# Kernel tuning notes

Measured on AMD Instinct MI355X. Metric: run time of the kernel, lower is better.

Reference implementation:

```python
import jax, jax.numpy as jnp
import numpy as np
from jax import lax

EPS = 1e-10
DELU_P = 10.0

def delu(x):
    # delu_feature_map: param*relu(x) + (exp(param*min(x,0)) - 1) + 1
    x1 = jax.nn.relu(x)
    x2 = jnp.exp(DELU_P * (x - x1)) - 1.0
    return DELU_P * x1 + x2 + 1.0

def conv1x1(x, w, b):
    # x: (B,C,H,W), w: (O,C), b: (O,)
    return jnp.einsum('bchw,oc->bohw', x, w) + b[None, :, None, None]

def conv3x3(x, w, b):
    # w: (O,I,3,3), SAME padding, stride 1
    y = lax.conv_general_dilated(x, w, window_strides=(1, 1), padding='SAME',
                                 dimension_numbers=('NCHW', 'OIHW', 'NCHW'))
    return y + b[None, :, None, None]

def setup_inputs() -> dict:
    key = jax.random.key(0)
    ks = jax.random.split(key, 12)
    B, C, H, W = 4, 256, 128, 128
    s = 0.02
    return {
        'x':   jax.random.normal(ks[0], (B, C, H, W), dtype=jnp.float32),
        'wq':  jax.random.normal(ks[1], (C, C), dtype=jnp.float32) * s,
        'bq':  jax.random.normal(ks[2], (C,), dtype=jnp.float32) * s,
        'wk':  jax.random.normal(ks[3], (C, C), dtype=jnp.float32) * s,
        'bk':  jax.random.normal(ks[4], (C,), dtype=jnp.float32) * s,
        'wv':  jax.random.normal(ks[5], (C, C), dtype=jnp.float32) * s,
        'bv':  jax.random.normal(ks[6], (C,), dtype=jnp.float32) * s,
        'wd1': jax.random.normal(ks[7], (C, C), dtype=jnp.float32) * s,
        'bd1': jax.random.normal(ks[8], (C,), dtype=jnp.float32) * s,
        'wd3': jax.random.normal(ks[9], (C, C, 3, 3), dtype=jnp.float32) * s,
        'bd3': jax.random.normal(ks[10], (C,), dtype=jnp.float32) * s,
        'gamma': jax.random.normal(ks[11], (1,), dtype=jnp.float32) * 0.1,
    }

def reference(x, wq, bq, wk, bk, wv, bv, wd1, bd1, wd3, bd3, gamma):
    B, C, H, W = x.shape
    N = H * W
    # q/k/v projections flattened to (B, C, N)
    q = conv1x1(x, wq, bq).reshape(B, C, N)
    k = conv1x1(x, wk, bk).reshape(B, C, N)
    v = conv1x1(x, wv, bv).reshape(B, C, N)
    # feature maps (torch permutes q to (B,N,C), applies map, permutes back -> elementwise, no-op layout)
    q = delu(q)
    k = delu(k)
    # energy: (B, C, C), contracting over spatial N (q indexed 'bmn')
    energy = jnp.einsum('bmn,bcn->bmc', q, k)
    KV = k * v  # (B, C, N) elementwise
    norm = 1.0 / (jnp.einsum('bmc,bcn->bn', energy, k) + EPS)  # (B, N)
    # attention: sum over m of energy, times KV, times norm -> (B, C, N)
    attention = jnp.einsum('bmc,bcn,bn->bcn', energy, KV, norm)
    out = attention.reshape(B, C, H, W)
    out = out + conv1x1(x, wd1, bd1) + conv3x3(x, wd3, bd3)
    return x + gamma[0] * out
```

## Files before the change

kernel.cpp:

```cpp
#include <hip/hip_runtime.h>
#include <hip/hip_fp8.h>

#define BB 4
#define CC 256
#define HH 128
#define WW 128
#define NN (HH*WW)
#define EPSF 1e-10f

#define XR 130
#define XPB ((size_t)XR*XR*CC)

typedef __bf16 bf16x8 __attribute__((ext_vector_type(8)));
typedef float  f32x4  __attribute__((ext_vector_type(4)));
typedef float  f32x16 __attribute__((ext_vector_type(16)));
typedef unsigned char uchar;

__device__ __forceinline__ float delu_f(float v) {
    return v > 0.0f ? fmaf(10.0f, v, 1.0f) : __expf(10.0f * v);
}

__device__ __forceinline__ uchar fp8b(float f) { return __hip_fp8_e4m3(f).__x; }
__device__ __forceinline__ float fp8f(uchar v) { __hip_fp8_e4m3 t; t.__x = v; return (float)t; }

__device__ __forceinline__ void gl_lds16(const void* g, void* l) {
    __builtin_amdgcn_global_load_lds(
        (const __attribute__((address_space(1))) void*)g,
        (__attribute__((address_space(3))) void*)l, 16, 0, 0);
}

__global__ __launch_bounds__(256) void k_prep(const float* __restrict__ wq,
    const float* __restrict__ wk, const float* __restrict__ wv,
    const float* __restrict__ wd1, const float* __restrict__ wd3,
    __bf16* __restrict__ wqb, __bf16* __restrict__ wkb, __bf16* __restrict__ wvb,
    uchar* __restrict__ wcv8)
{
    int idx = blockIdx.x * 256 + threadIdx.x;
    if (idx >= CC*CC) return;
    const int oc = idx >> 8, ic = idx & 255;
    const int ocf32 = oc >> 5;
    const int gks = ic >> 4, khi = (ic >> 3) & 1;
    const int lane32 = khi*32 + (oc & 31);
    const int e = ic & 7;
    const size_t off32 = ((size_t)(gks*8 + ocf32)*64 + lane32)*8 + e;
    wqb[off32] = (__bf16)wq[idx];
    wkb[off32] = (__bf16)wk[idx];
    wvb[off32] = (__bf16)wv[idx];
    float w9[9];
    #pragma unroll
    for (int k=0;k<9;k++) w9[k] = wd3[(size_t)idx*9 + k];
    w9[4] += wd1[idx];
    #pragma unroll
    for (int t=0;t<9;t++) wcv8[(size_t)t*CC*CC + off32] = fp8b(w9[t] * 16.0f);
}

__global__ __launch_bounds__(256) void k_halo(__bf16* __restrict__ xpad,
                                              uchar* __restrict__ xpad8)
{
    const int b = blockIdx.y;
    for (int t = blockIdx.x*256 + threadIdx.x; t < 516*32; t += 256*gridDim.x) {
        const int icg = t & 31;
        const int p   = t >> 5;
        int xrow, xcol;
        if (p < 260)      { xrow = (p < 130) ? 0 : 129; xcol = p % 130; }
        else              { int q = p - 260; xrow = 1 + (q >> 1); xcol = (q & 1) ? 129 : 0; }
        const size_t off = (size_t)b*XPB + ((size_t)xrow*XR + xcol)*CC + icg*8;
        *(bf16x8*)&xpad[off] = (bf16x8){};
        *(unsigned long long*)&xpad8[off] = 0ull;
    }
}

__global__ __launch_bounds__(256) void k_xpad(const float* __restrict__ x,
                                              __bf16* __restrict__ xpad,
                                              uchar* __restrict__ xpad8)
{
    __shared__ __bf16 tb[256*66];
    const int chunk = blockIdx.x;
    const int hr    = blockIdx.y;
    const int b     = blockIdx.z;
    const int tid   = threadIdx.x;
    const int wc0   = chunk*64;
    const float* xb = x + (size_t)b*CC*NN + (size_t)hr*WW + wc0;

    #pragma unroll
    for (int i = 0; i < 16; ++i) {
        const int ic  = i*16 + (tid >> 4);
        const int wcl = (tid & 15)*4;
        float4 v = *(const float4*)&xb[(size_t)ic*NN + wcl];
        __bf16* d = &tb[ic*66 + wcl];
        d[0] = (__bf16)v.x; d[1] = (__bf16)v.y; d[2] = (__bf16)v.z; d[3] = (__bf16)v.w;
    }
    __syncthreads();

    __bf16* xpb  = xpad  + (size_t)b*XPB + ((size_t)(hr+1)*XR + wc0 + 1)*CC;
    uchar*  xpb8 = xpad8 + (size_t)b*XPB + ((size_t)(hr+1)*XR + wc0 + 1)*CC;
    #pragma unroll
    for (int it = 0; it < 8; ++it) {
        const int o   = it*256 + tid;
        const int col = o >> 5;
        const int ic8 = (o & 31)*8;
        bf16x8 v;
        unsigned long long pk = 0;
        #pragma unroll
        for (int j = 0; j < 8; ++j) {
            __bf16 e = tb[(ic8 + j)*66 + col];
            v[j] = e;
            pk |= ((unsigned long long)fp8b((float)e)) << (8*j);
        }
        *(bf16x8*)&xpb[(size_t)col*CC + ic8] = v;
        *(unsigned long long*)&xpb8[(size_t)col*CC + ic8] = pk;
    }
}

__device__ __forceinline__ void stage_row128(const __bf16* __restrict__ xrb,
                                             __bf16* __restrict__ xs,
                                             int wid, int lane)
{
    #pragma unroll
    for (int j = 0; j < 16; ++j) {
        const int it = wid + 4*j;
        const int kq = it >> 1, ch = it & 1;
        gl_lds16(xrb + (size_t)(ch*64 + lane)*CC + kq*8, &xs[(size_t)(kq*132 + ch*64)*8]);
    }
}

__device__ __forceinline__ void mfma_gemm32(const __bf16* __restrict__ wb,
                                            const __bf16* __restrict__ xs,
                                            int wid, int lane, int l31, int lhi,
                                            f32x16 acc[2][4])
{
    #pragma unroll
    for (int kb=0; kb<8; kb++) {
        bf16x8 af[4];
        #pragma unroll
        for (int f=0; f<2; f++)
            #pragma unroll
            for (int kk=0; kk<2; kk++)
                af[f*2+kk] = *(const bf16x8*)&wb[((size_t)((kb*2+kk)*8 + wid*2 + f)*64 + lane)*8];
        #pragma unroll
        for (int kk=0; kk<2; kk++)
            #pragma unroll
            for (int nf=0; nf<4; nf++) {
                bf16x8 br = *(const bf16x8*)&xs[(size_t)((kb*4 + kk*2 + lhi)*132 + nf*32 + l31)*8];
                #pragma unroll
                for (int f=0; f<2; f++)
                    acc[f][nf] = __builtin_amdgcn_mfma_f32_32x32x16_bf16(af[f*2+kk], br, acc[f][nf], 0, 0, 0);
            }
    }
}

__global__ __launch_bounds__(256) void k_qk_mfma(const __bf16* __restrict__ xpad,
    const __bf16* __restrict__ wqb, const float* __restrict__ bq,
    const __bf16* __restrict__ wkb, const float* __restrict__ bk,
    uchar* __restrict__ kp8, float* __restrict__ Qs)
{
    __shared__ __bf16 xs[32*132*8];
    __shared__ float Qpart[4][128];
    const int h  = blockIdx.x;
    const int n0 = h * 128;
    const int b  = blockIdx.y;
    const int tid = threadIdx.x;
    const int wid = tid >> 6, lane = tid & 63;
    const int l31 = lane & 31, lhi = lane >> 5;
    const int oc_base = wid*64;
    const __bf16* xrb = xpad + (size_t)b*XPB + ((size_t)(h+1)*XR + 1)*CC;

    stage_row128(xrb, xs, wid, lane);
    __syncthreads();

    f32x16 acc[2][4] = {};
    mfma_gemm32(wqb, xs, wid, lane, l31, lhi, acc);
    #pragma unroll
    for (int nf=0; nf<4; nf++) {
        float s = 0.0f;
        #pragma unroll
        for (int f=0; f<2; f++)
            #pragma unroll
            for (int reg=0; reg<16; reg++) {
                const int oc = oc_base + f*32 + (reg&3) + 8*(reg>>2) + 4*lhi;
                s += delu_f(acc[f][nf][reg] + bq[oc]);
            }
        s += __shfl_xor(s, 32);
        if (lhi == 0) Qpart[wid][nf*32 + l31] = s;
    }
    __syncthreads();
    if (tid < 128)
        Qs[(size_t)b*NN + n0 + tid] = Qpart[0][tid] + Qpart[1][tid] + Qpart[2][tid] + Qpart[3][tid];

    #pragma unroll
    for (int f=0; f<2; f++)
        #pragma unroll
        for (int nf=0; nf<4; nf++)
            acc[f][nf] = (f32x16){};
    mfma_gemm32(wkb, xs, wid, lane, l31, lhi, acc);
    #pragma unroll
    for (int f=0; f<2; f++) {
        #pragma unroll
        for (int reg=0; reg<16; reg++) {
            const int oc = oc_base + f*32 + (reg&3) + 8*(reg>>2) + 4*lhi;
            const float bias = bk[oc];
            uchar* kr = kp8 + ((size_t)b*CC + oc)*NN + n0;
            #pragma unroll
            for (int nf=0; nf<4; nf++)
                kr[nf*32 + l31] = fp8b(delu_f(acc[f][nf][reg] + bias));
        }
    }
}

__global__ __launch_bounds__(256) void k_esum(const uchar* __restrict__ kp8,
    const float* __restrict__ Qs, float* __restrict__ Es)
{
    const int c = blockIdx.x & (CC-1), b = blockIdx.x >> 8;
    const int tid = threadIdx.x;
    const uchar* kr = kp8 + ((size_t)b*CC + c)*NN;
    const float4* qr = (const float4*)(Qs + (size_t)b*NN);
    float s = 0.0f;
    for (int i = tid; i < NN/8; i += 256) {
        unsigned long long kkb = *(const unsigned long long*)&kr[(size_t)i*8];
        float4 q0 = qr[2*i], q1 = qr[2*i+1];
        const float qv[8] = {q0.x,q0.y,q0.z,q0.w,q1.x,q1.y,q1.z,q1.w};
        #pragma unroll
        for (int j=0;j<8;j++)
            s = fmaf(fp8f((uchar)(kkb >> (8*j))), qv[j], s);
    }
    #pragma unroll
    for (int m=1; m<64; m<<=1) s += __shfl_xor(s, m, 64);
    __shared__ float red[4];
    if ((tid & 63) == 0) red[tid >> 6] = s;
    __syncthreads();
    if (tid == 0) Es[b*CC + c] = red[0] + red[1] + red[2] + red[3];
}

__global__ __launch_bounds__(256,2) void k_conv_mfma(const uchar* __restrict__ xpad8,
    const uchar* __restrict__ wcv8, const float* __restrict__ bd1,
    const float* __restrict__ bd3, __bf16* __restrict__ convout)
{
    __shared__ uchar xs8[2][6*132*16];
    const int orig = blockIdx.x;
    const int wg   = (orig & 7)*64 + (orig >> 3);
    const int b    = wg >> 7;
    const int h    = wg & 127;
    const int tid = threadIdx.x;
    const int wid = tid >> 6, lane = tid & 63;
    const int l31 = lane & 31, lhi = lane >> 5;
    const int oc_base = wid*64;
    const uchar* xpb8 = xpad8 + (size_t)b*XPB;

    f32x16 acc[2][4] = {};

    #define STAGE_CV8(bufsel, icb) do {                                         \
        const int ic0_ = (icb)*32;                                              \
        _Pragma("unroll")                                                       \
        for (int j = 0; j < 5; ++j) {                                           \
            const int w_ = wid + 4*j;                                           \
            if (w_ < 18) {                                                      \
                const int pair_ = w_ / 3, chunk_ = w_ % 3;                      \
                const int r_ = pair_ >> 1, g16_ = pair_ & 1;                    \
                const int col0_ = chunk_ * 64;                                  \
                if (col0_ + lane < XR)                                          \
                    gl_lds16(xpb8 + ((size_t)(h + r_)*XR + col0_ + lane)*CC + ic0_ + g16_*16, \
                             &xs8[bufsel][(size_t)(pair_*132 + col0_)*16]);     \
            }                                                                   \
        }                                                                       \
    } while (0)

    #define AF8_LOAD(dst, t, icb)                                               \
        _Pragma("unroll")                                                       \
        for (int f=0; f<2; f++)                                                 \
            _Pragma("unroll")                                                   \
            for (int kk=0; kk<2; kk++)                                          \
                dst[f*2+kk] = *(const long*)&wcv8[(size_t)(t)*CC*CC +           \
                    ((size_t)((((icb)*2 + kk)*8 + wid*2 + f))*64 + lane)*8];

    STAGE_CV8(0, 0);
    __syncthreads();

    #pragma unroll 1
    for (int icb = 0; icb < 8; ++icb) {
        long af8[2][4];
        AF8_LOAD(af8[0], 0, icb);
        if (icb < 7) STAGE_CV8((icb+1)&1, icb+1);
        #pragma unroll
        for (int t=0; t<9; ++t) {
            const int cur = t & 1, nxt = cur ^ 1;
            const int ky = t/3, kx = t%3;
            if (t < 8) { AF8_LOAD(af8[nxt], t+1, icb); }
            __builtin_amdgcn_s_setprio(1);
            #pragma unroll
            for (int kk=0; kk<2; kk++) {
                #pragma unroll
                for (int nf=0; nf<4; nf++) {
                    long br = *(const long*)&xs8[icb & 1][
                        (size_t)((ky*2 + kk)*132 + nf*32 + l31 + kx)*16 + lhi*8];
                    #pragma unroll
                    for (int f=0; f<2; f++)
                        acc[f][nf] = __builtin_amdgcn_mfma_f32_32x32x16_fp8_fp8(
                            af8[cur][f*2+kk], br, acc[f][nf], 0, 0, 0);
                }
            }
            __builtin_amdgcn_s_setprio(0);
        }
        __syncthreads();
    }
    #undef STAGE_CV8
    #undef AF8_LOAD

    #pragma unroll
    for (int f=0; f<2; f++) {
        #pragma unroll
        for (int reg=0; reg<16; reg++) {
            const int row = (reg & 3) + 8*(reg >> 2) + 4*lhi;
            const int oc = oc_base + f*32 + row;
            const float bias = bd1[oc] + bd3[oc];
            __bf16* orow = convout + ((size_t)b*CC + oc)*NN + (size_t)h*WW;
            #pragma unroll
            for (int nf=0; nf<4; nf++) {
                const int w = nf*32 + l31;
                orow[w] = (__bf16)(acc[f][nf][reg]*0.0625f + bias);
            }
        }
    }
}

__global__ __launch_bounds__(256) void k_vattn_mfma(
    const __bf16* __restrict__ xpad,
    const __bf16* __restrict__ wvb, const float* __restrict__ bv,
    const uchar* __restrict__ kp8, const float* __restrict__ Es,
    const __bf16* __restrict__ convout,
    const float* __restrict__ gamma, float* __restrict__ out)
{
    __shared__ __bf16 xs[32*132*8];
    __shared__ float Dpart[4][128];
    __shared__ float rn_sh[128];
    const int h  = blockIdx.x;
    const int n0 = h * 128;
    const int b  = blockIdx.y;
    const int tid = threadIdx.x;
    const int wid = tid >> 6, lane = tid & 63;
    const int l31 = lane & 31, lhi = lane >> 5;
    const int oc_base = wid*64;
    const __bf16* xrb = xpad + (size_t)b*XPB + ((size_t)(h+1)*XR + 1)*CC;

    stage_row128(xrb, xs, wid, lane);
    __syncthreads();

    f32x16 acc[2][4] = {};
    mfma_gemm32(wvb, xs, wid, lane, l31, lhi, acc);

    float dpart[4] = {0.f,0.f,0.f,0.f};
    #pragma unroll
    for (int f=0; f<2; f++) {
        #pragma unroll
        for (int reg=0; reg<16; reg++) {
            const int oc = oc_base + f*32 + (reg&3) + 8*(reg>>2) + 4*lhi;
            const float e = Es[b*CC + oc];
            const uchar* kr = kp8 + ((size_t)b*CC + oc)*NN + n0;
            #pragma unroll
            for (int nf=0; nf<4; nf++)
                dpart[nf] = fmaf(e, fp8f(kr[nf*32 + l31]), dpart[nf]);
        }
    }
    #pragma unroll
    for (int nf=0; nf<4; nf++) {
        dpart[nf] += __shfl_xor(dpart[nf], 32);
        if (lhi == 0) Dpart[wid][nf*32 + l31] = dpart[nf];
    }
    __syncthreads();
    if (tid < 128)
        rn_sh[tid] = 1.0f / (Dpart[0][tid] + Dpart[1][tid] + Dpart[2][tid] + Dpart[3][tid] + EPSF);
    __syncthreads();

    const float g = gamma[0];
    #pragma unroll
    for (int f=0; f<2; f++) {
        #pragma unroll
        for (int reg=0; reg<16; reg++) {
            const int oc = oc_base + f*32 + (reg&3) + 8*(reg>>2) + 4*lhi;
            const float eg = Es[b*CC + oc] * g;
            const float bias = bv[oc];
            const uchar*  kr = kp8 + ((size_t)b*CC + oc)*NN + n0;
            const __bf16* cr = convout + ((size_t)b*CC + oc)*NN + n0;
            const __bf16* xr = &xs[(size_t)((oc >> 3)*132)*8 + (oc & 7)];
            float* orow = out + ((size_t)b*CC + oc)*NN + n0;
            #pragma unroll
            for (int nf=0; nf<4; nf++) {
                const int w = nf*32 + l31;
                const float attn = eg*fp8f(kr[w])*rn_sh[w]*(acc[f][nf][reg] + bias);
                const float xv = (float)xr[(size_t)w*8];
                orow[w] = xv + attn + g*(float)cr[w];
            }
        }
    }
}

extern "C" void kernel_launch(void* const* d_in, const int* in_sizes, int n_in,
                              void* d_out, int out_size, void* d_ws, size_t ws_size,
                              hipStream_t stream)
{
    const float* x     = (const float*)d_in[0];
    const float* wq    = (const float*)d_in[1];
    const float* bq    = (const float*)d_in[2];
    const float* wk    = (const float*)d_in[3];
    const float* bk    = (const float*)d_in[4];
    const float* wv    = (const float*)d_in[5];
    const float* bv    = (const float*)d_in[6];
    const float* wd1   = (const float*)d_in[7];
    const float* bd1   = (const float*)d_in[8];
    const float* wd3   = (const float*)d_in[9];
    const float* bd3   = (const float*)d_in[10];
    const float* gamma = (const float*)d_in[11];
    float* out = (float*)d_out;

    uchar*  kp8   = (uchar*)d_ws;
    __bf16* cvout = (__bf16*)(kp8 + (size_t)BB*CC*NN);
    float*  Qs    = (float*)(cvout + (size_t)BB*CC*NN);
    float*  Es    = Qs + (size_t)BB*NN;
    uchar*  wcv8  = (uchar*)(Es + (size_t)BB*CC);
    __bf16* wqb   = (__bf16*)(wcv8 + (size_t)9*CC*CC);
    __bf16* wkb   = wqb + (size_t)CC*CC;
    __bf16* wvb   = wkb + (size_t)CC*CC;
    __bf16* xpad  = wvb + (size_t)CC*CC;
    uchar*  xpad8 = (uchar*)(xpad + (size_t)BB*XPB);

    k_prep      <<<dim3(CC*CC/256), 256, 0, stream>>>(wq, wk, wv, wd1, wd3, wqb, wkb, wvb, wcv8);
    k_halo      <<<dim3(16, BB), 256, 0, stream>>>(xpad, xpad8);
    k_xpad      <<<dim3(2, HH, BB), 256, 0, stream>>>(x, xpad, xpad8);
    k_qk_mfma   <<<dim3(HH, BB), 256, 0, stream>>>(xpad, wqb, bq, wkb, bk, kp8, Qs);
    k_esum      <<<dim3(BB*CC), 256, 0, stream>>>(kp8, Qs, Es);
    k_conv_mfma <<<dim3(HH*BB), 256, 0, stream>>>(xpad8, wcv8, bd1, bd3, cvout);
    k_vattn_mfma<<<dim3(HH, BB), 256, 0, stream>>>(xpad, wvb, bv, kp8, Es, cvout, gamma, out);
}
```

Before: 172.2 us.

## Fuse input transpose/padding into QK projection kernel

Removes the separate k_xpad kernel and has k_qk_mfma read fp32 x directly, convert it to bf16 in LDS in the layout the MFMA GEMM expects, and write the padded bf16 and fp8 copies from LDS for later kernels. This saves one launch and one re-read of the bf16 padded row from global memory. In exchange, the staging uses scattered 2-byte LDS stores that may cause bank conflicts, and it adds global write traffic inside the GEMM kernel.

```diff
diff --git a/kernel.cpp b/kernel.cpp
--- a/kernel.cpp
+++ b/kernel.cpp
@@ -70,48 +70,6 @@
     }
 }
 
-__global__ __launch_bounds__(256) void k_xpad(const float* __restrict__ x,
-                                              __bf16* __restrict__ xpad,
-                                              uchar* __restrict__ xpad8)
-{
-    __shared__ __bf16 tb[256*66];
-    const int chunk = blockIdx.x;
-    const int hr    = blockIdx.y;
-    const int b     = blockIdx.z;
-    const int tid   = threadIdx.x;
-    const int wc0   = chunk*64;
-    const float* xb = x + (size_t)b*CC*NN + (size_t)hr*WW + wc0;
-
-    #pragma unroll
-    for (int i = 0; i < 16; ++i) {
-        const int ic  = i*16 + (tid >> 4);
-        const int wcl = (tid & 15)*4;
-        float4 v = *(const float4*)&xb[(size_t)ic*NN + wcl];
-        __bf16* d = &tb[ic*66 + wcl];
-        d[0] = (__bf16)v.x; d[1] = (__bf16)v.y; d[2] = (__bf16)v.z; d[3] = (__bf16)v.w;
-    }
-    __syncthreads();
-
-    __bf16* xpb  = xpad  + (size_t)b*XPB + ((size_t)(hr+1)*XR + wc0 + 1)*CC;
-    uchar*  xpb8 = xpad8 + (size_t)b*XPB + ((size_t)(hr+1)*XR + wc0 + 1)*CC;
-    #pragma unroll
-    for (int it = 0; it < 8; ++it) {
-        const int o   = it*256 + tid;
-        const int col = o >> 5;
-        const int ic8 = (o & 31)*8;
-        bf16x8 v;
-        unsigned long long pk = 0;
-        #pragma unroll
-        for (int j = 0; j < 8; ++j) {
-            __bf16 e = tb[(ic8 + j)*66 + col];
-            v[j] = e;
-            pk |= ((unsigned long long)fp8b((float)e)) << (8*j);
-        }
-        *(bf16x8*)&xpb[(size_t)col*CC + ic8] = v;
-        *(unsigned long long*)&xpb8[(size_t)col*CC + ic8] = pk;
-    }
-}
-
 __device__ __forceinline__ void stage_row128(const __bf16* __restrict__ xrb,
                                              __bf16* __restrict__ xs,
                                              int wid, int lane)
@@ -149,10 +107,11 @@
     }
 }
 
-__global__ __launch_bounds__(256) void k_qk_mfma(const __bf16* __restrict__ xpad,
+__global__ __launch_bounds__(256) void k_qk_mfma(const float* __restrict__ x,
     const __bf16* __restrict__ wqb, const float* __restrict__ bq,
     const __bf16* __restrict__ wkb, const float* __restrict__ bk,
-    uchar* __restrict__ kp8, float* __restrict__ Qs)
+    uchar* __restrict__ kp8, float* __restrict__ Qs,
+    __bf16* __restrict__ xpad, uchar* __restrict__ xpad8)
 {
     __shared__ __bf16 xs[32*132*8];
     __shared__ float Qpart[4][128];
@@ -163,10 +122,40 @@
     const int wid = tid >> 6, lane = tid & 63;
     const int l31 = lane & 31, lhi = lane >> 5;
     const int oc_base = wid*64;
-    const __bf16* xrb = xpad + (size_t)b*XPB + ((size_t)(h+1)*XR + 1)*CC;
-
-    stage_row128(xrb, xs, wid, lane);
-    __syncthreads();
+
+    const float* xb = x + (size_t)b*CC*NN + (size_t)h*WW;
+    {
+        const int ic7 = tid & 7;
+        const int col = ((tid >> 3) & 31) * 4;
+        #pragma unroll
+        for (int i = 0; i < 32; ++i) {
+            const int ic = i*8 + ic7;
+            float4 v = *(const float4*)&xb[(size_t)ic*NN + col];
+            const int b0 = (i*132 + col)*8 + ic7;
+            xs[b0]      = (__bf16)v.x;
+            xs[b0 + 8]  = (__bf16)v.y;
+            xs[b0 + 16] = (__bf16)v.z;
+            xs[b0 + 24] = (__bf16)v.w;
+        }
+    }
+    __syncthreads();
+
+    {
+        __bf16* xpb  = xpad  + (size_t)b*XPB + ((size_t)(h+1)*XR + 1)*CC;
+        uchar*  xpb8 = xpad8 + (size_t)b*XPB + ((size_t)(h+1)*XR + 1)*CC;
+        #pragma unroll
+        for (int it = 0; it < 16; ++it) {
+            const int o   = it*256 + tid;
+            const int col = o >> 5, kq = o & 31;
+            bf16x8 v = *(const bf16x8*)&xs[(size_t)(kq*132 + col)*8];
+            unsigned long long pk = 0;
+            #pragma unroll
+            for (int j = 0; j < 8; ++j)
+                pk |= ((unsigned long long)fp8b((float)v[j])) << (8*j);
+            *(bf16x8*)&xpb[(size_t)col*CC + kq*8] = v;
+            *(unsigned long long*)&xpb8[(size_t)col*CC + kq*8] = pk;
+        }
+    }
 
     f32x16 acc[2][4] = {};
     mfma_gemm32(wqb, xs, wid, lane, l31, lhi, acc);
@@ -424,8 +413,7 @@
 
     k_prep      <<<dim3(CC*CC/256), 256, 0, stream>>>(wq, wk, wv, wd1, wd3, wqb, wkb, wvb, wcv8);
     k_halo      <<<dim3(16, BB), 256, 0, stream>>>(xpad, xpad8);
-    k_xpad      <<<dim3(2, HH, BB), 256, 0, stream>>>(x, xpad, xpad8);
-    k_qk_mfma   <<<dim3(HH, BB), 256, 0, stream>>>(xpad, wqb, bq, wkb, bk, kp8, Qs);
+    k_qk_mfma   <<<dim3(HH, BB), 256, 0, stream>>>(x, wqb, bq, wkb, bk, kp8, Qs, xpad, xpad8);
     k_esum      <<<dim3(BB*CC), 256, 0, stream>>>(kp8, Qs, Es);
     k_conv_mfma <<<dim3(HH*BB), 256, 0, stream>>>(xpad8, wcv8, bd1, bd3, cvout);
     k_vattn_mfma<<<dim3(HH, BB), 256, 0, stream>>>(xpad, wvb, bv, kp8, Es, cvout, gamma, out);
```

Result: faster. 164.7 us (-4.4%).
